# Kernel optimization log

Measured on AMD Instinct MI355X. Metric: run time of the kernel, lower is better.

The kernel has to match this reference:

```python
import jax, jax.numpy as jnp
import numpy as np

HIDDEN = 1024
HEADS = 16
HEAD_DIM = HIDDEN // HEADS
B, S = 2, 1024


def setup_inputs() -> dict:
    key = jax.random.key(0)
    ks = jax.random.split(key, 14)
    sc = 1.0 / np.sqrt(HIDDEN)
    inp = {
        "q": jax.random.normal(ks[0], (B, S, HIDDEN), jnp.float32),
        "k": jax.random.normal(ks[1], (B, S, HIDDEN), jnp.float32),
        "v": jax.random.normal(ks[2], (B, S, HIDDEN), jnp.float32),
        "mask": jax.random.randint(ks[3], (B, S), 0, 2, jnp.int32),
        "shift": jax.random.normal(ks[4], (B * HEADS, S, S), jnp.float32) * 0.1,
        "wq": jax.random.normal(ks[5], (HIDDEN, HIDDEN), jnp.float32) * sc,
        "bq": jnp.zeros((HIDDEN,), jnp.float32),
        "wk": jax.random.normal(ks[6], (HIDDEN, HIDDEN), jnp.float32) * sc,
        "bk": jnp.zeros((HIDDEN,), jnp.float32),
        "wv": jax.random.normal(ks[7], (HIDDEN, HIDDEN), jnp.float32) * sc,
        "bv": jnp.zeros((HIDDEN,), jnp.float32),
        "wo": jax.random.normal(ks[8], (HIDDEN, HIDDEN), jnp.float32) * sc,
        "bo": jnp.zeros((HIDDEN,), jnp.float32),
    }
    return inp


def _to_heads(x):
    # (B,S,Dm) -> (B*H, S, Dh), batch-major over heads (b*H + h)
    b, s, _ = x.shape
    return x.reshape(b, s, HEADS, HEAD_DIM).transpose(0, 2, 1, 3).reshape(b * HEADS, s, HEAD_DIM)


def reference(q, k, v, mask, shift, wq, bq, wk, bk, wv, bv, wo, bo):
    b, s, dm = q.shape
    qh = _to_heads(q @ wq.T + bq)
    kh = _to_heads(k @ wk.T + bk)
    vh = _to_heads(v @ wv.T + bv)
    scores = jnp.einsum("bqd,bkd->bqk", qh, kh) / jnp.float32(np.sqrt(HEAD_DIM))
    scores = scores + shift
    # faithful to torch: mask tiled head-major (h*B + b) -> outer product m_i * m_j
    m = jnp.tile(mask, (HEADS, 1))  # (H*B, S)
    attn_mask = m[:, :, None] * m[:, None, :]  # (H*B, S, S)
    scores = jnp.where(attn_mask == 0, jnp.float32(-1e9), scores)
    p = jax.nn.softmax(scores, axis=-1)
    out = jnp.einsum("bqk,bkd->bqd", p, vh)
    out = out.reshape(b, HEADS, s, HEAD_DIM).transpose(0, 2, 1, 3).reshape(b, s, dm)
    return out @ wo.T + bo
```

## Files before the change

kernel.cpp:

```cpp
#include <hip/hip_runtime.h>
#include <hip/hip_bf16.h>

#define S_LEN 1024
#define DMODEL 1024
#define N_HEADS 16
#define D_HEAD 64
#define BATCH 2
#define N_BH 32

typedef __attribute__((ext_vector_type(8))) short short8;
typedef __attribute__((ext_vector_type(4))) float f32x4;
typedef __attribute__((ext_vector_type(4))) int i32x4;

static __device__ __forceinline__ unsigned short f2bf(float x) {
    unsigned int u = __float_as_uint(x);
    return (unsigned short)((u + 0x7fffu + ((u >> 16) & 1u)) >> 16);
}

static __device__ __forceinline__ f32x4 ldnt4(const float* p) {
    return __builtin_nontemporal_load(reinterpret_cast<const f32x4*>(p));
}

template <int AMODE>
__device__ __forceinline__ void gemm_body(const void* __restrict__ Araw,
                                          const float* __restrict__ W,
                                          const float* __restrict__ bias,
                                          void* __restrict__ outp, int outmode,
                                          int n0, int j0)
{
    __shared__ unsigned short As[128 * 40];
    __shared__ unsigned short Bs[64 * 40];
    const int t = threadIdx.x;
    const int lane = t & 63, w = t >> 6;
    const int wm = w >> 1, wn = w & 1;
    const int g = lane >> 4, r = lane & 15;

    f32x4 acc[4][2];
#pragma unroll
    for (int mi = 0; mi < 4; ++mi)
#pragma unroll
        for (int ni = 0; ni < 2; ++ni)
            acc[mi][ni] = (f32x4){0.f, 0.f, 0.f, 0.f};

    for (int ks = 0; ks < DMODEL / 32; ++ks) {
        const int k0 = ks * 32;
        __syncthreads();
        if (AMODE == 0) {
            const float* A = (const float*)Araw;
#pragma unroll
            for (int i = 0; i < 4; ++i) {
                int row = (t >> 3) + i * 32;
                int quad = t & 7;
                float4 f = *reinterpret_cast<const float4*>(A + (size_t)(n0 + row) * DMODEL + k0 + quad * 4);
                ushort4 hv = { f2bf(f.x), f2bf(f.y), f2bf(f.z), f2bf(f.w) };
                *reinterpret_cast<ushort4*>(&As[row * 40 + quad * 4]) = hv;
            }
        } else {
            const unsigned short* A = (const unsigned short*)Araw;
#pragma unroll
            for (int i = 0; i < 2; ++i) {
                int row = (t >> 2) + i * 64;
                int seg = t & 3;
                short8 v8 = *reinterpret_cast<const short8*>(A + (size_t)(n0 + row) * DMODEL + k0 + seg * 8);
                *reinterpret_cast<short8*>(&As[row * 40 + seg * 8]) = v8;
            }
        }
#pragma unroll
        for (int i = 0; i < 2; ++i) {
            int row = (t >> 3) + i * 32;
            int quad = t & 7;
            float4 f = *reinterpret_cast<const float4*>(W + (size_t)(j0 + row) * DMODEL + k0 + quad * 4);
            ushort4 hv = { f2bf(f.x), f2bf(f.y), f2bf(f.z), f2bf(f.w) };
            *reinterpret_cast<ushort4*>(&Bs[row * 40 + quad * 4]) = hv;
        }
        __syncthreads();
        short8 af[4], bfr[2];
#pragma unroll
        for (int mi = 0; mi < 4; ++mi)
            af[mi] = *reinterpret_cast<const short8*>(&As[(wm * 64 + mi * 16 + r) * 40 + g * 8]);
#pragma unroll
        for (int ni = 0; ni < 2; ++ni)
            bfr[ni] = *reinterpret_cast<const short8*>(&Bs[(wn * 32 + ni * 16 + r) * 40 + g * 8]);
#pragma unroll
        for (int mi = 0; mi < 4; ++mi)
#pragma unroll
            for (int ni = 0; ni < 2; ++ni)
                acc[mi][ni] = __builtin_amdgcn_mfma_f32_16x16x32_bf16(af[mi], bfr[ni], acc[mi][ni], 0, 0, 0);
    }

#pragma unroll
    for (int mi = 0; mi < 4; ++mi) {
#pragma unroll
        for (int ni = 0; ni < 2; ++ni) {
            int col = j0 + wn * 32 + ni * 16 + r;
            float bv = bias[col];
#pragma unroll
            for (int t4 = 0; t4 < 4; ++t4) {
                int n = n0 + wm * 64 + mi * 16 + g * 4 + t4;
                float v = acc[mi][ni][t4] + bv;
                if (outmode == 2) {
                    ((float*)outp)[(size_t)n * DMODEL + col] = v;
                } else {
                    int b_ = n >> 10, s_ = n & 1023;
                    int h_ = col >> 6, dh = col & 63;
                    if (outmode == 0)
                        ((unsigned short*)outp)[((size_t)(b_ * N_HEADS + h_) * S_LEN + s_) * D_HEAD + dh] = f2bf(v);
                    else
                        ((unsigned short*)outp)[((size_t)(b_ * N_HEADS + h_) * D_HEAD + dh) * S_LEN + s_] = f2bf(v);
                }
            }
        }
    }
}

__global__ __launch_bounds__(256) void qkv_kernel(
    const float* __restrict__ qx, const float* __restrict__ kx, const float* __restrict__ vx,
    const float* __restrict__ wq, const float* __restrict__ wk, const float* __restrict__ wv,
    const float* __restrict__ bq, const float* __restrict__ bk, const float* __restrict__ bv,
    unsigned short* Qh, unsigned short* Kh, unsigned short* Vt)
{
    const int z = blockIdx.z;
    const float* A    = (z == 0) ? qx : (z == 1) ? kx : vx;
    const float* W    = (z == 0) ? wq : (z == 1) ? wk : wv;
    const float* bias = (z == 0) ? bq : (z == 1) ? bk : bv;
    void* outp = (z == 0) ? (void*)Qh : (z == 1) ? (void*)Kh : (void*)Vt;
    gemm_body<0>(A, W, bias, outp, (z == 2) ? 1 : 0, blockIdx.x * 128, blockIdx.y * 64);
}

__global__ __launch_bounds__(256) void oproj_kernel(
    const unsigned short* __restrict__ attn, const float* __restrict__ wo,
    const float* __restrict__ bo, float* out)
{
    gemm_body<1>(attn, wo, bo, (void*)out, 2, blockIdx.x * 128, blockIdx.y * 64);
}

__global__ __launch_bounds__(256) void attn_kernel(
    const unsigned short* __restrict__ Qh, const unsigned short* __restrict__ Kh,
    const unsigned short* __restrict__ Vt, const int* __restrict__ mask,
    const float* __restrict__ shift, unsigned short* __restrict__ attnbuf)
{
    __shared__ __align__(16) char smem[17408];
    __shared__ float Lw[4][16];
    auto Plds = reinterpret_cast<unsigned short(*)[16][72]>(smem);
    auto Olds = reinterpret_cast<float(*)[16][68]>(smem);

    const int qg = blockIdx.x, bh = blockIdx.y;
    const int b_ = bh >> 4, h_ = bh & 15;
    const int t = threadIdx.x, w = t >> 6, lane = t & 63;
    const int g = lane >> 4, r = lane & 15;
    const int q0 = qg * 16;
    const int kstart = w * 256;

    const unsigned short* Qb = Qh + (size_t)bh * S_LEN * D_HEAD;
    const unsigned short* Kb = Kh + (size_t)bh * S_LEN * D_HEAD;
    const unsigned short* Vb = Vt + (size_t)bh * D_HEAD * S_LEN;
    const float* shb = shift + (size_t)bh * S_LEN * S_LEN;
    const int* mp = mask + (bh & (BATCH - 1)) * S_LEN;

    short8 qf0 = *reinterpret_cast<const short8*>(&Qb[(size_t)(q0 + r) * D_HEAD + g * 8]);
    short8 qf1 = *reinterpret_cast<const short8*>(&Qb[(size_t)(q0 + r) * D_HEAD + 32 + g * 8]);
    const int mq = mp[q0 + r];
    const size_t shrow = (size_t)(q0 + r) * S_LEN;

    float l_loc = 0.f;
    f32x4 o_acc[4];
#pragma unroll
    for (int i = 0; i < 4; ++i) o_acc[i] = (f32x4){0.f, 0.f, 0.f, 0.f};

    f32x4 sh[4];
#pragma unroll
    for (int fn = 0; fn < 4; ++fn)
        sh[fn] = ldnt4(shb + shrow + kstart + fn * 16 + g * 4);

#pragma unroll
    for (int kt = 0; kt < 4; ++kt) {
        const int kbase = kstart + kt * 64;
        f32x4 shc[4];
#pragma unroll
        for (int fn = 0; fn < 4; ++fn) shc[fn] = sh[fn];
        if (kt < 3) {
#pragma unroll
            for (int fn = 0; fn < 4; ++fn)
                sh[fn] = ldnt4(shb + shrow + kbase + 64 + fn * 16 + g * 4);
        }

        short8 kf[8];
#pragma unroll
        for (int fn = 0; fn < 4; ++fn) {
            kf[2 * fn]     = *reinterpret_cast<const short8*>(&Kb[(size_t)(kbase + fn * 16 + r) * D_HEAD + g * 8]);
            kf[2 * fn + 1] = *reinterpret_cast<const short8*>(&Kb[(size_t)(kbase + fn * 16 + r) * D_HEAD + 32 + g * 8]);
        }

        float pexp[4][4];
#pragma unroll
        for (int fn = 0; fn < 4; ++fn) {
            f32x4 a = (f32x4){0.f, 0.f, 0.f, 0.f};
            a = __builtin_amdgcn_mfma_f32_16x16x32_bf16(kf[2 * fn], qf0, a, 0, 0, 0);
            a = __builtin_amdgcn_mfma_f32_16x16x32_bf16(kf[2 * fn + 1], qf1, a, 0, 0, 0);
            i32x4 mk = *reinterpret_cast<const i32x4*>(mp + kbase + fn * 16 + g * 4);
#pragma unroll
            for (int t4 = 0; t4 < 4; ++t4) {
                float e = __expf(fmaf(a[t4], 0.125f, shc[fn][t4]));
                float p = (mq & mk[t4]) ? e : 0.0f;
                if (mq == 0) p = 1.0f;
                pexp[fn][t4] = p;
                l_loc += p;
            }
        }

        short8 vfa[8];
#pragma unroll
        for (int df = 0; df < 4; ++df) {
            vfa[2 * df]     = *reinterpret_cast<const short8*>(&Vb[(size_t)(df * 16 + r) * S_LEN + kbase + g * 8]);
            vfa[2 * df + 1] = *reinterpret_cast<const short8*>(&Vb[(size_t)(df * 16 + r) * S_LEN + kbase + 32 + g * 8]);
        }

#pragma unroll
        for (int fn = 0; fn < 4; ++fn) {
            ushort4 pk = { f2bf(pexp[fn][0]), f2bf(pexp[fn][1]), f2bf(pexp[fn][2]), f2bf(pexp[fn][3]) };
            *reinterpret_cast<ushort4*>(&Plds[w][r][fn * 16 + g * 4]) = pk;
        }
        asm volatile("s_waitcnt lgkmcnt(0)" ::: "memory");
        __builtin_amdgcn_sched_barrier(0);
        short8 pf0 = *reinterpret_cast<const short8*>(&Plds[w][r][g * 8]);
        short8 pf1 = *reinterpret_cast<const short8*>(&Plds[w][r][32 + g * 8]);
#pragma unroll
        for (int df = 0; df < 4; ++df) {
            o_acc[df] = __builtin_amdgcn_mfma_f32_16x16x32_bf16(pf0, vfa[2 * df], o_acc[df], 0, 0, 0);
            o_acc[df] = __builtin_amdgcn_mfma_f32_16x16x32_bf16(pf1, vfa[2 * df + 1], o_acc[df], 0, 0, 0);
        }
    }

    l_loc += __shfl_xor(l_loc, 16);
    l_loc += __shfl_xor(l_loc, 32);

    __syncthreads();

    if (g == 0) Lw[w][r] = l_loc;
#pragma unroll
    for (int df = 0; df < 4; ++df)
#pragma unroll
        for (int t4 = 0; t4 < 4; ++t4)
            Olds[w][g * 4 + t4][df * 16 + r] = o_acc[df][t4];

    __syncthreads();

    {
        const int col = t & 63;
        const int rb = t >> 6;
#pragma unroll
        for (int i = 0; i < 4; ++i) {
            int row = rb * 4 + i;
            float L = Lw[0][row] + Lw[1][row] + Lw[2][row] + Lw[3][row];
            float o = Olds[0][row][col] + Olds[1][row][col] + Olds[2][row][col] + Olds[3][row][col];
            attnbuf[(size_t)(b_ * S_LEN + q0 + row) * DMODEL + h_ * D_HEAD + col] = f2bf(o / L);
        }
    }
}

extern "C" void kernel_launch(void* const* d_in, const int* in_sizes, int n_in,
                              void* d_out, int out_size, void* d_ws, size_t ws_size,
                              hipStream_t stream)
{
    const float* q     = (const float*)d_in[0];
    const float* k     = (const float*)d_in[1];
    const float* v     = (const float*)d_in[2];
    const int*   mask  = (const int*)d_in[3];
    const float* shift = (const float*)d_in[4];
    const float* wq    = (const float*)d_in[5];
    const float* bq    = (const float*)d_in[6];
    const float* wk    = (const float*)d_in[7];
    const float* bk    = (const float*)d_in[8];
    const float* wv    = (const float*)d_in[9];
    const float* bv    = (const float*)d_in[10];
    const float* wo    = (const float*)d_in[11];
    const float* bo    = (const float*)d_in[12];
    float* out = (float*)d_out;

    const size_t nhalf = (size_t)N_BH * S_LEN * D_HEAD;
    unsigned short* Qh = (unsigned short*)d_ws;
    unsigned short* Kh = Qh + nhalf;
    unsigned short* Vt = Kh + nhalf;
    unsigned short* attnbuf = Vt + nhalf;

    dim3 blk(256);
    qkv_kernel<<<dim3(16, 16, 3), blk, 0, stream>>>(q, k, v, wq, wk, wv, bq, bk, bv, Qh, Kh, Vt);
    attn_kernel<<<dim3(64, 32), blk, 0, stream>>>(Qh, Kh, Vt, mask, shift, attnbuf);
    oproj_kernel<<<dim3(16, 16), blk, 0, stream>>>(attnbuf, wo, bo, out);
}
```

Measured before the change: 156.2 us.

## Raise attention occupancy, interleave K/V loads, and remap blocks across XCDs

Adds a min-blocks-per-CU launch bound of 8 to the attention kernel. It restructures the per-tile loop so K fragments are loaded and consumed per sub-tile, and V fragments are loaded right before their MFMA, which cuts live registers. The 2D grid becomes a 1D grid of 2048 blocks with a swizzle (f&7)*256+(f>>3), so consecutive blocks on the same XCD share a head's K/V in L2. The trade-off is less load latency hiding inside each wave, and possible spills if the register cap is too tight.

```diff
diff --git a/kernel.cpp b/kernel.cpp
--- a/kernel.cpp
+++ b/kernel.cpp
@@ -134,7 +134,7 @@
     gemm_body<1>(attn, wo, bo, (void*)out, 2, blockIdx.x * 128, blockIdx.y * 64);
 }
 
-__global__ __launch_bounds__(256) void attn_kernel(
+__global__ __launch_bounds__(256, 8) void attn_kernel(
     const unsigned short* __restrict__ Qh, const unsigned short* __restrict__ Kh,
     const unsigned short* __restrict__ Vt, const int* __restrict__ mask,
     const float* __restrict__ shift, unsigned short* __restrict__ attnbuf)
@@ -144,7 +144,9 @@
     auto Plds = reinterpret_cast<unsigned short(*)[16][72]>(smem);
     auto Olds = reinterpret_cast<float(*)[16][68]>(smem);
 
-    const int qg = blockIdx.x, bh = blockIdx.y;
+    const int f = blockIdx.x;
+    const int l = (f & 7) * 256 + (f >> 3);
+    const int bh = l >> 6, qg = l & 63;
     const int b_ = bh >> 4, h_ = bh & 15;
     const int t = threadIdx.x, w = t >> 6, lane = t & 63;
     const int g = lane >> 4, r = lane & 15;
@@ -175,59 +177,48 @@
 #pragma unroll
     for (int kt = 0; kt < 4; ++kt) {
         const int kbase = kstart + kt * 64;
-        f32x4 shc[4];
-#pragma unroll
-        for (int fn = 0; fn < 4; ++fn) shc[fn] = sh[fn];
+
+#pragma unroll
+        for (int fn = 0; fn < 4; ++fn) {
+            short8 kv0 = *reinterpret_cast<const short8*>(&Kb[(size_t)(kbase + fn * 16 + r) * D_HEAD + g * 8]);
+            short8 kv1 = *reinterpret_cast<const short8*>(&Kb[(size_t)(kbase + fn * 16 + r) * D_HEAD + 32 + g * 8]);
+            f32x4 a = (f32x4){0.f, 0.f, 0.f, 0.f};
+            a = __builtin_amdgcn_mfma_f32_16x16x32_bf16(kv0, qf0, a, 0, 0, 0);
+            a = __builtin_amdgcn_mfma_f32_16x16x32_bf16(kv1, qf1, a, 0, 0, 0);
+            i32x4 mk = *reinterpret_cast<const i32x4*>(mp + kbase + fn * 16 + g * 4);
+            float p0, p1, p2, p3;
+            {
+                float e0 = __expf(fmaf(a[0], 0.125f, sh[fn][0]));
+                float e1 = __expf(fmaf(a[1], 0.125f, sh[fn][1]));
+                float e2 = __expf(fmaf(a[2], 0.125f, sh[fn][2]));
+                float e3 = __expf(fmaf(a[3], 0.125f, sh[fn][3]));
+                p0 = (mq & mk[0]) ? e0 : 0.f;
+                p1 = (mq & mk[1]) ? e1 : 0.f;
+                p2 = (mq & mk[2]) ? e2 : 0.f;
+                p3 = (mq & mk[3]) ? e3 : 0.f;
+                if (mq == 0) { p0 = p1 = p2 = p3 = 1.f; }
+            }
+            l_loc += (p0 + p1) + (p2 + p3);
+            ushort4 pk = { f2bf(p0), f2bf(p1), f2bf(p2), f2bf(p3) };
+            *reinterpret_cast<ushort4*>(&Plds[w][r][fn * 16 + g * 4]) = pk;
+        }
+
         if (kt < 3) {
 #pragma unroll
             for (int fn = 0; fn < 4; ++fn)
                 sh[fn] = ldnt4(shb + shrow + kbase + 64 + fn * 16 + g * 4);
         }
 
-        short8 kf[8];
-#pragma unroll
-        for (int fn = 0; fn < 4; ++fn) {
-            kf[2 * fn]     = *reinterpret_cast<const short8*>(&Kb[(size_t)(kbase + fn * 16 + r) * D_HEAD + g * 8]);
-            kf[2 * fn + 1] = *reinterpret_cast<const short8*>(&Kb[(size_t)(kbase + fn * 16 + r) * D_HEAD + 32 + g * 8]);
-        }
-
-        float pexp[4][4];
-#pragma unroll
-        for (int fn = 0; fn < 4; ++fn) {
-            f32x4 a = (f32x4){0.f, 0.f, 0.f, 0.f};
-            a = __builtin_amdgcn_mfma_f32_16x16x32_bf16(kf[2 * fn], qf0, a, 0, 0, 0);
-            a = __builtin_amdgcn_mfma_f32_16x16x32_bf16(kf[2 * fn + 1], qf1, a, 0, 0, 0);
-            i32x4 mk = *reinterpret_cast<const i32x4*>(mp + kbase + fn * 16 + g * 4);
-#pragma unroll
-            for (int t4 = 0; t4 < 4; ++t4) {
-                float e = __expf(fmaf(a[t4], 0.125f, shc[fn][t4]));
-                float p = (mq & mk[t4]) ? e : 0.0f;
-                if (mq == 0) p = 1.0f;
-                pexp[fn][t4] = p;
-                l_loc += p;
-            }
-        }
-
-        short8 vfa[8];
-#pragma unroll
-        for (int df = 0; df < 4; ++df) {
-            vfa[2 * df]     = *reinterpret_cast<const short8*>(&Vb[(size_t)(df * 16 + r) * S_LEN + kbase + g * 8]);
-            vfa[2 * df + 1] = *reinterpret_cast<const short8*>(&Vb[(size_t)(df * 16 + r) * S_LEN + kbase + 32 + g * 8]);
-        }
-
-#pragma unroll
-        for (int fn = 0; fn < 4; ++fn) {
-            ushort4 pk = { f2bf(pexp[fn][0]), f2bf(pexp[fn][1]), f2bf(pexp[fn][2]), f2bf(pexp[fn][3]) };
-            *reinterpret_cast<ushort4*>(&Plds[w][r][fn * 16 + g * 4]) = pk;
-        }
         asm volatile("s_waitcnt lgkmcnt(0)" ::: "memory");
         __builtin_amdgcn_sched_barrier(0);
         short8 pf0 = *reinterpret_cast<const short8*>(&Plds[w][r][g * 8]);
         short8 pf1 = *reinterpret_cast<const short8*>(&Plds[w][r][32 + g * 8]);
 #pragma unroll
         for (int df = 0; df < 4; ++df) {
-            o_acc[df] = __builtin_amdgcn_mfma_f32_16x16x32_bf16(pf0, vfa[2 * df], o_acc[df], 0, 0, 0);
-            o_acc[df] = __builtin_amdgcn_mfma_f32_16x16x32_bf16(pf1, vfa[2 * df + 1], o_acc[df], 0, 0, 0);
+            short8 vf0 = *reinterpret_cast<const short8*>(&Vb[(size_t)(df * 16 + r) * S_LEN + kbase + g * 8]);
+            short8 vf1 = *reinterpret_cast<const short8*>(&Vb[(size_t)(df * 16 + r) * S_LEN + kbase + 32 + g * 8]);
+            o_acc[df] = __builtin_amdgcn_mfma_f32_16x16x32_bf16(pf0, vf0, o_acc[df], 0, 0, 0);
+            o_acc[df] = __builtin_amdgcn_mfma_f32_16x16x32_bf16(pf1, vf1, o_acc[df], 0, 0, 0);
         }
     }
 
@@ -285,6 +276,6 @@
 
     dim3 blk(256);
     qkv_kernel<<<dim3(16, 16, 3), blk, 0, stream>>>(q, k, v, wq, wk, wv, bq, bk, bv, Qh, Kh, Vt);
-    attn_kernel<<<dim3(64, 32), blk, 0, stream>>>(Qh, Kh, Vt, mask, shift, attnbuf);
+    attn_kernel<<<dim3(2048), blk, 0, stream>>>(Qh, Kh, Vt, mask, shift, attnbuf);
     oproj_kernel<<<dim3(16, 16), blk, 0, stream>>>(attnbuf, wo, bo, out);
 }
```

Result: slower. 220.8 us (+41.4%).

## Split fused attention into materialized score kernel and PV GEMM kernel

Applied to the files above, without the earlier changes.

Replaces the single fused attention kernel with two kernels. A score kernel computes QK^T tiles, applies shift, mask and exp, then writes bf16 probabilities to a workspace score buffer. A PV kernel then tiles P·V and row-sums P for normalization. Launches are chunked over heads according to workspace size. This trades the fused kernel's per-warp structure for GEMM-style tiling, at the cost of writing and re-reading a 2-byte-per-element score matrix and possibly many launches.

```diff
diff --git a/kernel.cpp b/kernel.cpp
--- a/kernel.cpp
+++ b/kernel.cpp
@@ -17,8 +17,15 @@
     return (unsigned short)((u + 0x7fffu + ((u >> 16) & 1u)) >> 16);
 }
 
-static __device__ __forceinline__ f32x4 ldnt4(const float* p) {
-    return __builtin_nontemporal_load(reinterpret_cast<const f32x4*>(p));
+static __device__ __forceinline__ float bf2f(unsigned short h) {
+    return __uint_as_float(((unsigned int)h) << 16);
+}
+
+static __device__ __forceinline__ float sum8(short8 v) {
+    float s = 0.f;
+#pragma unroll
+    for (int j = 0; j < 8; ++j) s += bf2f((unsigned short)v[j]);
+    return s;
 }
 
 template <int AMODE>
@@ -134,128 +141,163 @@
     gemm_body<1>(attn, wo, bo, (void*)out, 2, blockIdx.x * 128, blockIdx.y * 64);
 }
 
-__global__ __launch_bounds__(256) void attn_kernel(
+__global__ __launch_bounds__(256) void score_kernel(
     const unsigned short* __restrict__ Qh, const unsigned short* __restrict__ Kh,
-    const unsigned short* __restrict__ Vt, const int* __restrict__ mask,
-    const float* __restrict__ shift, unsigned short* __restrict__ attnbuf)
-{
-    __shared__ __align__(16) char smem[17408];
-    __shared__ float Lw[4][16];
-    auto Plds = reinterpret_cast<unsigned short(*)[16][72]>(smem);
-    auto Olds = reinterpret_cast<float(*)[16][68]>(smem);
-
-    const int qg = blockIdx.x, bh = blockIdx.y;
-    const int b_ = bh >> 4, h_ = bh & 15;
-    const int t = threadIdx.x, w = t >> 6, lane = t & 63;
-    const int g = lane >> 4, r = lane & 15;
-    const int q0 = qg * 16;
-    const int kstart = w * 256;
-
+    const int* __restrict__ mask, const float* __restrict__ shift,
+    unsigned short* __restrict__ Sbuf, int bh0)
+{
+    __shared__ union {
+        struct { unsigned short As[128 * 72]; unsigned short Bs[64 * 72]; } st;
+        float C[128 * 68];
+    } u;
+    const int zloc = blockIdx.z;
+    const int bh = bh0 + zloc;
+    const int q0 = blockIdx.x * 128, j0 = blockIdx.y * 64;
+    const int t = threadIdx.x, lane = t & 63, w = t >> 6;
+    const int wm = w >> 1, wn = w & 1, g = lane >> 4, r = lane & 15;
     const unsigned short* Qb = Qh + (size_t)bh * S_LEN * D_HEAD;
     const unsigned short* Kb = Kh + (size_t)bh * S_LEN * D_HEAD;
+    unsigned short* Sl = Sbuf + (size_t)zloc * S_LEN * S_LEN;
+    const int* mrow = mask + (bh & (BATCH - 1)) * S_LEN;
+
+    {
+        int row = t >> 3, seg = t & 7;
+#pragma unroll
+        for (int i = 0; i < 4; ++i)
+            *reinterpret_cast<short8*>(&u.st.As[(row + i * 32) * 72 + seg * 8]) =
+                *reinterpret_cast<const short8*>(Qb + (size_t)(q0 + row + i * 32) * D_HEAD + seg * 8);
+#pragma unroll
+        for (int i = 0; i < 2; ++i)
+            *reinterpret_cast<short8*>(&u.st.Bs[(row + i * 32) * 72 + seg * 8]) =
+                *reinterpret_cast<const short8*>(Kb + (size_t)(j0 + row + i * 32) * D_HEAD + seg * 8);
+    }
+    __syncthreads();
+
+    f32x4 acc[4][2];
+#pragma unroll
+    for (int mi = 0; mi < 4; ++mi)
+#pragma unroll
+        for (int ni = 0; ni < 2; ++ni)
+            acc[mi][ni] = (f32x4){0.f, 0.f, 0.f, 0.f};
+
+#pragma unroll
+    for (int ks = 0; ks < 2; ++ks) {
+        short8 af[4], bf[2];
+#pragma unroll
+        for (int mi = 0; mi < 4; ++mi)
+            af[mi] = *reinterpret_cast<const short8*>(&u.st.As[(wm * 64 + mi * 16 + r) * 72 + ks * 32 + g * 8]);
+#pragma unroll
+        for (int ni = 0; ni < 2; ++ni)
+            bf[ni] = *reinterpret_cast<const short8*>(&u.st.Bs[(wn * 32 + ni * 16 + r) * 72 + ks * 32 + g * 8]);
+#pragma unroll
+        for (int mi = 0; mi < 4; ++mi)
+#pragma unroll
+            for (int ni = 0; ni < 2; ++ni)
+                acc[mi][ni] = __builtin_amdgcn_mfma_f32_16x16x32_bf16(af[mi], bf[ni], acc[mi][ni], 0, 0, 0);
+    }
+    __syncthreads();
+
+#pragma unroll
+    for (int mi = 0; mi < 4; ++mi)
+#pragma unroll
+        for (int ni = 0; ni < 2; ++ni)
+#pragma unroll
+            for (int t4 = 0; t4 < 4; ++t4)
+                u.C[(wm * 64 + mi * 16 + g * 4 + t4) * 68 + wn * 32 + ni * 16 + r] = acc[mi][ni][t4];
+    __syncthreads();
+
+#pragma unroll
+    for (int c = 0; c < 8; ++c) {
+        int flat = c * 1024 + t * 4;
+        int row = flat >> 6;
+        int col = flat & 63;
+        f32x4 cv = *reinterpret_cast<const f32x4*>(&u.C[row * 68 + col]);
+        f32x4 sv = *reinterpret_cast<const f32x4*>(
+            shift + ((size_t)bh * S_LEN + q0 + row) * S_LEN + j0 + col);
+        i32x4 mk = *reinterpret_cast<const i32x4*>(mrow + j0 + col);
+        int mq = mrow[q0 + row];
+        float p0 = (mq & mk[0]) ? __expf(fmaf(cv[0], 0.125f, sv[0])) : 0.f;
+        float p1 = (mq & mk[1]) ? __expf(fmaf(cv[1], 0.125f, sv[1])) : 0.f;
+        float p2 = (mq & mk[2]) ? __expf(fmaf(cv[2], 0.125f, sv[2])) : 0.f;
+        float p3 = (mq & mk[3]) ? __expf(fmaf(cv[3], 0.125f, sv[3])) : 0.f;
+        if (mq == 0) { p0 = p1 = p2 = p3 = 1.f; }
+        ushort4 pk = { f2bf(p0), f2bf(p1), f2bf(p2), f2bf(p3) };
+        *reinterpret_cast<ushort4*>(Sl + (size_t)(q0 + row) * S_LEN + j0 + col) = pk;
+    }
+}
+
+__global__ __launch_bounds__(256) void pv_kernel(
+    const unsigned short* __restrict__ Sbuf, const unsigned short* __restrict__ Vt,
+    unsigned short* __restrict__ attnbuf, int bh0)
+{
+    __shared__ unsigned short Ss[64 * 72];
+    __shared__ unsigned short Vs[64 * 72];
+    __shared__ float Lsum[64];
+    const int zloc = blockIdx.y;
+    const int bh = bh0 + zloc;
+    const int q0 = blockIdx.x * 64;
+    const int b_ = bh >> 4, h_ = bh & 15;
+    const int t = threadIdx.x, lane = t & 63, w = t >> 6;
+    const int wm = w >> 1, wn = w & 1, g = lane >> 4, r = lane & 15;
+    const unsigned short* Sl = Sbuf + (size_t)zloc * S_LEN * S_LEN;
     const unsigned short* Vb = Vt + (size_t)bh * D_HEAD * S_LEN;
-    const float* shb = shift + (size_t)bh * S_LEN * S_LEN;
-    const int* mp = mask + (bh & (BATCH - 1)) * S_LEN;
-
-    short8 qf0 = *reinterpret_cast<const short8*>(&Qb[(size_t)(q0 + r) * D_HEAD + g * 8]);
-    short8 qf1 = *reinterpret_cast<const short8*>(&Qb[(size_t)(q0 + r) * D_HEAD + 32 + g * 8]);
-    const int mq = mp[q0 + r];
-    const size_t shrow = (size_t)(q0 + r) * S_LEN;
-
-    float l_loc = 0.f;
-    f32x4 o_acc[4];
-#pragma unroll
-    for (int i = 0; i < 4; ++i) o_acc[i] = (f32x4){0.f, 0.f, 0.f, 0.f};
-
-    f32x4 sh[4];
-#pragma unroll
-    for (int fn = 0; fn < 4; ++fn)
-        sh[fn] = ldnt4(shb + shrow + kstart + fn * 16 + g * 4);
-
-#pragma unroll
-    for (int kt = 0; kt < 4; ++kt) {
-        const int kbase = kstart + kt * 64;
-        f32x4 shc[4];
-#pragma unroll
-        for (int fn = 0; fn < 4; ++fn) shc[fn] = sh[fn];
-        if (kt < 3) {
-#pragma unroll
-            for (int fn = 0; fn < 4; ++fn)
-                sh[fn] = ldnt4(shb + shrow + kbase + 64 + fn * 16 + g * 4);
+    const int srow = t >> 3, seg = t & 7;
+
+    float rs0 = 0.f, rs1 = 0.f;
+    f32x4 acc[2][2];
+#pragma unroll
+    for (int mi = 0; mi < 2; ++mi)
+#pragma unroll
+        for (int ni = 0; ni < 2; ++ni)
+            acc[mi][ni] = (f32x4){0.f, 0.f, 0.f, 0.f};
+
+    for (int kt = 0; kt < 16; ++kt) {
+        const int k0 = kt * 64;
+        __syncthreads();
+        short8 sv0 = *reinterpret_cast<const short8*>(Sl + (size_t)(q0 + srow) * S_LEN + k0 + seg * 8);
+        short8 sv1 = *reinterpret_cast<const short8*>(Sl + (size_t)(q0 + srow + 32) * S_LEN + k0 + seg * 8);
+        short8 vv0 = *reinterpret_cast<const short8*>(Vb + (size_t)srow * S_LEN + k0 + seg * 8);
+        short8 vv1 = *reinterpret_cast<const short8*>(Vb + (size_t)(srow + 32) * S_LEN + k0 + seg * 8);
+        *reinterpret_cast<short8*>(&Ss[srow * 72 + seg * 8]) = sv0;
+        *reinterpret_cast<short8*>(&Ss[(srow + 32) * 72 + seg * 8]) = sv1;
+        *reinterpret_cast<short8*>(&Vs[srow * 72 + seg * 8]) = vv0;
+        *reinterpret_cast<short8*>(&Vs[(srow + 32) * 72 + seg * 8]) = vv1;
+        rs0 += sum8(sv0);
+        rs1 += sum8(sv1);
+        __syncthreads();
+#pragma unroll
+        for (int ks = 0; ks < 2; ++ks) {
+            short8 af[2], bf[2];
+#pragma unroll
+            for (int mi = 0; mi < 2; ++mi)
+                af[mi] = *reinterpret_cast<const short8*>(&Ss[(wm * 32 + mi * 16 + r) * 72 + ks * 32 + g * 8]);
+#pragma unroll
+            for (int ni = 0; ni < 2; ++ni)
+                bf[ni] = *reinterpret_cast<const short8*>(&Vs[(wn * 32 + ni * 16 + r) * 72 + ks * 32 + g * 8]);
+#pragma unroll
+            for (int mi = 0; mi < 2; ++mi)
+#pragma unroll
+                for (int ni = 0; ni < 2; ++ni)
+                    acc[mi][ni] = __builtin_amdgcn_mfma_f32_16x16x32_bf16(af[mi], bf[ni], acc[mi][ni], 0, 0, 0);
         }
-
-        short8 kf[8];
-#pragma unroll
-        for (int fn = 0; fn < 4; ++fn) {
-            kf[2 * fn]     = *reinterpret_cast<const short8*>(&Kb[(size_t)(kbase + fn * 16 + r) * D_HEAD + g * 8]);
-            kf[2 * fn + 1] = *reinterpret_cast<const short8*>(&Kb[(size_t)(kbase + fn * 16 + r) * D_HEAD + 32 + g * 8]);
-        }
-
-        float pexp[4][4];
-#pragma unroll
-        for (int fn = 0; fn < 4; ++fn) {
-            f32x4 a = (f32x4){0.f, 0.f, 0.f, 0.f};
-            a = __builtin_amdgcn_mfma_f32_16x16x32_bf16(kf[2 * fn], qf0, a, 0, 0, 0);
-            a = __builtin_amdgcn_mfma_f32_16x16x32_bf16(kf[2 * fn + 1], qf1, a, 0, 0, 0);
-            i32x4 mk = *reinterpret_cast<const i32x4*>(mp + kbase + fn * 16 + g * 4);
+    }
+
+    rs0 += __shfl_xor(rs0, 1); rs0 += __shfl_xor(rs0, 2); rs0 += __shfl_xor(rs0, 4);
+    rs1 += __shfl_xor(rs1, 1); rs1 += __shfl_xor(rs1, 2); rs1 += __shfl_xor(rs1, 4);
+    if (seg == 0) { Lsum[srow] = rs0; Lsum[srow + 32] = rs1; }
+    __syncthreads();
+
+#pragma unroll
+    for (int mi = 0; mi < 2; ++mi)
+#pragma unroll
+        for (int ni = 0; ni < 2; ++ni)
 #pragma unroll
             for (int t4 = 0; t4 < 4; ++t4) {
-                float e = __expf(fmaf(a[t4], 0.125f, shc[fn][t4]));
-                float p = (mq & mk[t4]) ? e : 0.0f;
-                if (mq == 0) p = 1.0f;
-                pexp[fn][t4] = p;
-                l_loc += p;
+                int row = wm * 32 + mi * 16 + g * 4 + t4;
+                int col = wn * 32 + ni * 16 + r;
+                float o = acc[mi][ni][t4] / Lsum[row];
+                attnbuf[((size_t)(b_ * S_LEN + q0 + row)) * DMODEL + h_ * D_HEAD + col] = f2bf(o);
             }
-        }
-
-        short8 vfa[8];
-#pragma unroll
-        for (int df = 0; df < 4; ++df) {
-            vfa[2 * df]     = *reinterpret_cast<const short8*>(&Vb[(size_t)(df * 16 + r) * S_LEN + kbase + g * 8]);
-            vfa[2 * df + 1] = *reinterpret_cast<const short8*>(&Vb[(size_t)(df * 16 + r) * S_LEN + kbase + 32 + g * 8]);
-        }
-
-#pragma unroll
-        for (int fn = 0; fn < 4; ++fn) {
-            ushort4 pk = { f2bf(pexp[fn][0]), f2bf(pexp[fn][1]), f2bf(pexp[fn][2]), f2bf(pexp[fn][3]) };
-            *reinterpret_cast<ushort4*>(&Plds[w][r][fn * 16 + g * 4]) = pk;
-        }
-        asm volatile("s_waitcnt lgkmcnt(0)" ::: "memory");
-        __builtin_amdgcn_sched_barrier(0);
-        short8 pf0 = *reinterpret_cast<const short8*>(&Plds[w][r][g * 8]);
-        short8 pf1 = *reinterpret_cast<const short8*>(&Plds[w][r][32 + g * 8]);
-#pragma unroll
-        for (int df = 0; df < 4; ++df) {
-            o_acc[df] = __builtin_amdgcn_mfma_f32_16x16x32_bf16(pf0, vfa[2 * df], o_acc[df], 0, 0, 0);
-            o_acc[df] = __builtin_amdgcn_mfma_f32_16x16x32_bf16(pf1, vfa[2 * df + 1], o_acc[df], 0, 0, 0);
-        }
-    }
-
-    l_loc += __shfl_xor(l_loc, 16);
-    l_loc += __shfl_xor(l_loc, 32);
-
-    __syncthreads();
-
-    if (g == 0) Lw[w][r] = l_loc;
-#pragma unroll
-    for (int df = 0; df < 4; ++df)
-#pragma unroll
-        for (int t4 = 0; t4 < 4; ++t4)
-            Olds[w][g * 4 + t4][df * 16 + r] = o_acc[df][t4];
-
-    __syncthreads();
-
-    {
-        const int col = t & 63;
-        const int rb = t >> 6;
-#pragma unroll
-        for (int i = 0; i < 4; ++i) {
-            int row = rb * 4 + i;
-            float L = Lw[0][row] + Lw[1][row] + Lw[2][row] + Lw[3][row];
-            float o = Olds[0][row][col] + Olds[1][row][col] + Olds[2][row][col] + Olds[3][row][col];
-            attnbuf[(size_t)(b_ * S_LEN + q0 + row) * DMODEL + h_ * D_HEAD + col] = f2bf(o / L);
-        }
-    }
 }
 
 extern "C" void kernel_launch(void* const* d_in, const int* in_sizes, int n_in,
@@ -282,9 +324,22 @@
     unsigned short* Kh = Qh + nhalf;
     unsigned short* Vt = Kh + nhalf;
     unsigned short* attnbuf = Vt + nhalf;
+    unsigned short* Sbuf = attnbuf + (size_t)BATCH * S_LEN * DMODEL;
+
+    const size_t base16 = 16u * 1024 * 1024;
+    const size_t sbytes = (size_t)S_LEN * S_LEN * 2;
+    int CH = 1;
+    if (ws_size > base16) {
+        size_t c = (ws_size - base16) / sbytes;
+        CH = (c >= 32) ? 32 : (c < 1 ? 1 : (int)c);
+    }
 
     dim3 blk(256);
     qkv_kernel<<<dim3(16, 16, 3), blk, 0, stream>>>(q, k, v, wq, wk, wv, bq, bk, bv, Qh, Kh, Vt);
-    attn_kernel<<<dim3(64, 32), blk, 0, stream>>>(Qh, Kh, Vt, mask, shift, attnbuf);
+    for (int bh0 = 0; bh0 < N_BH; bh0 += CH) {
+        int c = (N_BH - bh0 < CH) ? (N_BH - bh0) : CH;
+        score_kernel<<<dim3(8, 16, c), blk, 0, stream>>>(Qh, Kh, mask, shift, Sbuf, bh0);
+        pv_kernel<<<dim3(16, c), blk, 0, stream>>>(Sbuf, Vt, attnbuf, bh0);
+    }
     oproj_kernel<<<dim3(16, 16), blk, 0, stream>>>(attnbuf, wo, bo, out);
 }
```

New measurement: 133.2 us. 14.7% less time.
